# Kernel tuning notes

Measured on AMD Instinct MI355X. Metric: run time of the kernel, lower is better.

Reference implementation:

```python
import jax, jax.numpy as jnp
import numpy as np

VOCAB = 256
EMBED = 128
HIDDEN = 512
BATCH = 64
SEQ = 1024


def setup_inputs() -> dict:
    key = jax.random.key(0)
    ks = jax.random.split(key, 6)
    x = jax.random.randint(ks[0], (BATCH, SEQ), 0, VOCAB)
    hidden = jnp.zeros((BATCH, HIDDEN), dtype=jnp.float32)
    embedding = jax.random.normal(ks[1], (VOCAB, EMBED), dtype=jnp.float32)
    W_xh = jax.random.normal(ks[2], (EMBED, HIDDEN), dtype=jnp.float32) * 0.01
    W_hh = jax.random.normal(ks[3], (HIDDEN, HIDDEN), dtype=jnp.float32) * 0.01
    b_h = jnp.zeros((HIDDEN,), dtype=jnp.float32)
    # nn.Linear(hidden, vocab): weight [vocab, hidden], bias [vocab]
    W_hy_w = jax.random.normal(ks[4], (VOCAB, HIDDEN), dtype=jnp.float32) * (1.0 / np.sqrt(HIDDEN))
    W_hy_b = jax.random.normal(ks[5], (VOCAB,), dtype=jnp.float32) * 0.01
    return {"x": x, "hidden": hidden, "embedding": embedding, "W_xh": W_xh,
            "W_hh": W_hh, "b_h": b_h, "W_hy_w": W_hy_w, "W_hy_b": W_hy_b}


def reference(x, hidden, embedding, W_xh, W_hh, b_h, W_hy_w, W_hy_b):
    # x: [b, l] int tokens -> embed: [b, l, e]
    x_embed = embedding[x]
    # Precompute input projections in one batched GEMM: [l, b, h]
    xw = jnp.einsum('ble,eh->lbh', x_embed, W_xh) + b_h

    def step(h, xw_t):
        h_new = jnp.tanh(xw_t + h @ W_hh)
        return h_new, h_new

    final_hidden, outs = jax.lax.scan(step, hidden, xw)  # outs: [l, b, h]
    outs = jnp.transpose(outs, (1, 0, 2))  # [b, l, h]
    logits = outs @ W_hy_w.T + W_hy_b  # [b, l, vocab]
    return logits, final_hidden
```

## Files before the change

kernel.cpp:

```cpp
#include <hip/hip_runtime.h>
#include <hip/hip_bf16.h>
#include <stdint.h>

#define BATCH  64
#define SEQ    1024
#define EMBED  128
#define HIDDEN 512
#define VOCAB  256

using bf16 = __hip_bfloat16;
typedef __attribute__((ext_vector_type(8))) short bf16x8;
typedef __attribute__((ext_vector_type(4))) float f32x4;

__device__ __forceinline__ float bfu(unsigned short u) {
    return __uint_as_float(((unsigned)u) << 16);
}

__global__ void k_cvt(const float* __restrict__ in, bf16* __restrict__ out, int n) {
    int i = blockIdx.x * 256 + threadIdx.x;
    if (i < n) out[i] = __float2bfloat16(in[i]);
}

__global__ void k_txp_wxh(const float* __restrict__ in, bf16* __restrict__ out) {
    int idx = blockIdx.x * 256 + threadIdx.x;
    int e = idx >> 9, j = idx & 511;
    out[j * EMBED + e] = __float2bfloat16(in[idx]);
}

__global__ void k_txp_whh(const float* __restrict__ in, bf16* __restrict__ out) {
    int idx = blockIdx.x * 256 + threadIdx.x;
    int k = idx >> 9, n = idx & 511;
    out[n * HIDDEN + k] = __float2bfloat16(in[idx]);
}

template<bool GATHER, bool OUT_BF16>
__global__ __launch_bounds__(256) void k_gemm(
    const bf16* __restrict__ A,
    const int*  __restrict__ xtok,
    const bf16* __restrict__ B,
    const float* __restrict__ bias,
    float* __restrict__ Cf,
    bf16*  __restrict__ Cb,
    int M, int N, int K)
{
    __shared__ bf16 As[64][72];
    __shared__ bf16 Bs[64][72];
    const int m0 = blockIdx.x * 64, n0 = blockIdx.y * 64;
    const int tid  = threadIdx.x;
    const int lane = tid & 63, wid = tid >> 6;
    const int wm = wid >> 1, wn = wid & 1;
    const int lrow = tid >> 3, lc8 = tid & 7;

    f32x4 acc[2][2] = {};

    for (int k0 = 0; k0 < K; k0 += 64) {
#pragma unroll
        for (int pass = 0; pass < 2; ++pass) {
            int row = pass * 32 + lrow;
            const bf16* asrc;
            if (GATHER) {
                int m = m0 + row;
                int t = m >> 6, bb = m & 63;
                int tok = xtok[bb * SEQ + t];
                asrc = A + (size_t)tok * K + k0 + lc8 * 8;
            } else {
                asrc = A + (size_t)(m0 + row) * K + k0 + lc8 * 8;
            }
            *reinterpret_cast<uint4*>(&As[row][lc8 * 8]) = *reinterpret_cast<const uint4*>(asrc);
            *reinterpret_cast<uint4*>(&Bs[row][lc8 * 8]) =
                *reinterpret_cast<const uint4*>(B + (size_t)(n0 + row) * K + k0 + lc8 * 8);
        }
        __syncthreads();
#pragma unroll
        for (int kk = 0; kk < 2; ++kk) {
            bf16x8 af[2], bg[2];
#pragma unroll
            for (int mt = 0; mt < 2; ++mt)
                af[mt] = *reinterpret_cast<const bf16x8*>(
                    &As[wm * 32 + mt * 16 + (lane & 15)][kk * 32 + (lane >> 4) * 8]);
#pragma unroll
            for (int nt = 0; nt < 2; ++nt)
                bg[nt] = *reinterpret_cast<const bf16x8*>(
                    &Bs[wn * 32 + nt * 16 + (lane & 15)][kk * 32 + (lane >> 4) * 8]);
#pragma unroll
            for (int mt = 0; mt < 2; ++mt)
#pragma unroll
                for (int nt = 0; nt < 2; ++nt)
                    acc[mt][nt] = __builtin_amdgcn_mfma_f32_16x16x32_bf16(
                        af[mt], bg[nt], acc[mt][nt], 0, 0, 0);
        }
        __syncthreads();
    }
#pragma unroll
    for (int mt = 0; mt < 2; ++mt) {
        int rbase = m0 + wm * 32 + mt * 16 + (lane >> 4) * 4;
#pragma unroll
        for (int nt = 0; nt < 2; ++nt) {
            int col = n0 + wn * 32 + nt * 16 + (lane & 15);
            float bv = bias[col];
#pragma unroll
            for (int r = 0; r < 4; ++r) {
                float v = acc[mt][nt][r] + bv;
                size_t off = (size_t)(rbase + r) * N + col;
                if (OUT_BF16) Cb[off] = __float2bfloat16(v);
                else          Cf[off] = v;
            }
        }
    }
}

#define ROWS 16
#define CHK_LDS 3
#define CHK_REG 8
#define WRES_STRIDE (CHK_LDS * 32 + 8)
#define H_STRIDE (HIDDEN + 8)

__global__ __launch_bounds__(512, 2) void k_scan_mfma(
    const bf16* __restrict__ xwb,
    const bf16* __restrict__ wt,
    const float* __restrict__ h0,
    bf16* __restrict__ hh,
    float* __restrict__ hfin)
{
    __shared__ bf16 wres[HIDDEN * WRES_STRIDE];
    __shared__ bf16 h_lds[2][ROWS * H_STRIDE];

    const int tid  = threadIdx.x;
    const int lane = tid & 63, wid = tid >> 6;
    const int b0   = blockIdx.x * ROWS;
    const int scol = wid * 64;
    const int lm   = lane & 15, lk = lane >> 4;

    {
        const bf16* src = wt + (size_t)tid * HIDDEN;
        bf16* dst = &wres[tid * WRES_STRIDE];
#pragma unroll
        for (int j = 0; j < (CHK_LDS * 32) / 8; ++j)
            *reinterpret_cast<uint4*>(dst + j * 8) =
                *reinterpret_cast<const uint4*>(src + j * 8);
    }
    {
        int row = tid >> 5, c = (tid & 31) * 16;
        const float* src = h0 + (size_t)(b0 + row) * HIDDEN + c;
        bf16 tmp[16];
#pragma unroll
        for (int j = 0; j < 16; ++j) tmp[j] = __float2bfloat16(src[j]);
        *reinterpret_cast<uint4*>(&h_lds[0][row * H_STRIDE + c])     = *reinterpret_cast<uint4*>(&tmp[0]);
        *reinterpret_cast<uint4*>(&h_lds[0][row * H_STRIDE + c + 8]) = *reinterpret_cast<uint4*>(&tmp[8]);
    }

    bf16x8 breg[CHK_REG][4];
#pragma unroll
    for (int c = 0; c < CHK_REG; ++c)
#pragma unroll
        for (int nt = 0; nt < 4; ++nt)
            breg[c][nt] = *reinterpret_cast<const bf16x8*>(
                wt + (size_t)(scol + nt * 16 + lm) * HIDDEN + (CHK_LDS + c) * 32 + lk * 8);

    const bf16* grow[4];
    const bf16* lrow[4];
#pragma unroll
    for (int nt = 0; nt < 4; ++nt) {
        int row = scol + nt * 16 + lm;
        grow[nt] = wt + (size_t)row * HIDDEN + lk * 8;
        lrow[nt] = &wres[row * WRES_STRIDE + lk * 8];
    }

    __syncthreads();

    int p = 0;
    for (int t = 0; t < SEQ; ++t) {
        const ushort* xbase = reinterpret_cast<const ushort*>(
            xwb + ((size_t)t * BATCH + b0) * HIDDEN);
        ushort xwv[4][4];
#pragma unroll
        for (int nt = 0; nt < 4; ++nt)
#pragma unroll
            for (int r = 0; r < 4; ++r)
                xwv[nt][r] = xbase[(size_t)(lk * 4 + r) * HIDDEN + scol + nt * 16 + lm];

        f32x4 acc[4] = {};
#pragma unroll
        for (int kc = 0; kc < 16; ++kc) {
            bf16x8 af = *reinterpret_cast<const bf16x8*>(
                &h_lds[p][lm * H_STRIDE + kc * 32 + lk * 8]);
#pragma unroll
            for (int nt = 0; nt < 4; ++nt) {
                bf16x8 bg;
                if (kc < CHK_LDS)
                    bg = *reinterpret_cast<const bf16x8*>(lrow[nt] + kc * 32);
                else if (kc < CHK_LDS + CHK_REG)
                    bg = breg[kc - CHK_LDS][nt];
                else
                    bg = *reinterpret_cast<const bf16x8*>(grow[nt] + kc * 32);
                acc[nt] = __builtin_amdgcn_mfma_f32_16x16x32_bf16(af, bg, acc[nt], 0, 0, 0);
            }
        }

#pragma unroll
        for (int nt = 0; nt < 4; ++nt) {
            int col = scol + nt * 16 + lm;
#pragma unroll
            for (int r = 0; r < 4; ++r) {
                int m = lk * 4 + r;
                float pre = acc[nt][r] + bfu(xwv[nt][r]);
                float e2  = __expf(2.f * pre);
                float hn  = 1.f - 2.f / (e2 + 1.f);
                bf16 hb   = __float2bfloat16(hn);
                h_lds[p ^ 1][m * H_STRIDE + col] = hb;
                hh[((size_t)(b0 + m) * SEQ + t) * HIDDEN + col] = hb;
                if (t == SEQ - 1) hfin[(size_t)(b0 + m) * HIDDEN + col] = hn;
            }
        }
        p ^= 1;
        __syncthreads();
    }
}

extern "C" void kernel_launch(void* const* d_in, const int* in_sizes, int n_in,
                              void* d_out, int out_size, void* d_ws, size_t ws_size,
                              hipStream_t stream) {
    const int*   x    = (const int*)  d_in[0];
    const float* h0   = (const float*)d_in[1];
    const float* emb  = (const float*)d_in[2];
    const float* wxh  = (const float*)d_in[3];
    const float* whh  = (const float*)d_in[4];
    const float* bh   = (const float*)d_in[5];
    const float* whyw = (const float*)d_in[6];
    const float* whyb = (const float*)d_in[7];

    float* logits = (float*)d_out;
    float* hfin   = logits + (size_t)BATCH * SEQ * VOCAB;

    char* p = (char*)d_ws;
    bf16* xwb    = (bf16*)p; p += (size_t)SEQ * BATCH * HIDDEN * 2;
    bf16* hh     = (bf16*)p; p += (size_t)BATCH * SEQ * HIDDEN * 2;
    bf16* wt     = (bf16*)p; p += (size_t)HIDDEN * HIDDEN * 2;
    bf16* wxh_t  = (bf16*)p; p += (size_t)HIDDEN * EMBED * 2;
    bf16* emb_bf = (bf16*)p; p += (size_t)VOCAB * EMBED * 2;
    bf16* why_bf = (bf16*)p; p += (size_t)VOCAB * HIDDEN * 2;

    k_txp_whh<<<(HIDDEN * HIDDEN + 255) / 256, 256, 0, stream>>>(whh, wt);
    k_cvt<<<(VOCAB * EMBED + 255) / 256, 256, 0, stream>>>(emb, emb_bf, VOCAB * EMBED);
    k_cvt<<<(VOCAB * HIDDEN + 255) / 256, 256, 0, stream>>>(whyw, why_bf, VOCAB * HIDDEN);
    k_txp_wxh<<<(EMBED * HIDDEN + 255) / 256, 256, 0, stream>>>(wxh, wxh_t);

    k_gemm<true, true><<<dim3((SEQ * BATCH) / 64, HIDDEN / 64), 256, 0, stream>>>(
        emb_bf, x, wxh_t, bh, nullptr, xwb, SEQ * BATCH, HIDDEN, EMBED);

    k_scan_mfma<<<BATCH / ROWS, 512, 0, stream>>>(xwb, wt, h0, hh, hfin);

    k_gemm<false, false><<<dim3((BATCH * SEQ) / 64, VOCAB / 64), 256, 0, stream>>>(
        hh, nullptr, why_bf, whyb, logits, nullptr, BATCH * SEQ, VOCAB, HIDDEN);
}
```

Baseline: 3.171 ms.

## Permute xw layout for per-thread vector loads and defer coalesced hh stores

The input-projection GEMM now writes its bf16 output in a permuted layout, so each scan thread loads its 16 xw values with two 16-byte loads instead of 16 scattered 2-byte loads. The scan no longer stores each hidden element straight to global memory. Instead it copies the previous step's h from LDS to hh with wide coalesced stores at the start of the next step, plus one final flush after the loop. An empty asm barrier is also added to keep the register-resident weight chunks pinned. This targets the latency-bound serial recurrence by cutting per-step global memory instructions, at the cost of extra LDS reads and a layout tied to the fixed shapes.

```diff
diff --git a/kernel.cpp b/kernel.cpp
--- a/kernel.cpp
+++ b/kernel.cpp
@@ -33,7 +33,7 @@
     out[n * HIDDEN + k] = __float2bfloat16(in[idx]);
 }
 
-template<bool GATHER, bool OUT_BF16>
+template<bool GATHER, bool OUT_BF16, bool PERMUTE>
 __global__ __launch_bounds__(256) void k_gemm(
     const bf16* __restrict__ A,
     const int*  __restrict__ xtok,
@@ -91,19 +91,38 @@
         }
         __syncthreads();
     }
-#pragma unroll
-    for (int mt = 0; mt < 2; ++mt) {
-        int rbase = m0 + wm * 32 + mt * 16 + (lane >> 4) * 4;
-#pragma unroll
-        for (int nt = 0; nt < 2; ++nt) {
-            int col = n0 + wn * 32 + nt * 16 + (lane & 15);
-            float bv = bias[col];
-#pragma unroll
-            for (int r = 0; r < 4; ++r) {
-                float v = acc[mt][nt][r] + bv;
-                size_t off = (size_t)(rbase + r) * N + col;
-                if (OUT_BF16) Cb[off] = __float2bfloat16(v);
-                else          Cf[off] = v;
+    if (PERMUTE) {
+        const int t = m0 >> 6, wid_s = n0 >> 6;
+#pragma unroll
+        for (int mt = 0; mt < 2; ++mt) {
+            int blk = wm * 2 + mt;
+            bf16 tmp[8];
+#pragma unroll
+            for (int nt = 0; nt < 2; ++nt) {
+                int col = n0 + wn * 32 + nt * 16 + (lane & 15);
+                float bv = bias[col];
+#pragma unroll
+                for (int r = 0; r < 4; ++r)
+                    tmp[nt * 4 + r] = __float2bfloat16(acc[mt][nt][r] + bv);
+            }
+            size_t off = (((size_t)(t * 4 + blk) * 512) + wid_s * 64 + lane) * 16 + wn * 8;
+            *reinterpret_cast<uint4*>(Cb + off) = *reinterpret_cast<uint4*>(tmp);
+        }
+    } else {
+#pragma unroll
+        for (int mt = 0; mt < 2; ++mt) {
+            int rbase = m0 + wm * 32 + mt * 16 + (lane >> 4) * 4;
+#pragma unroll
+            for (int nt = 0; nt < 2; ++nt) {
+                int col = n0 + wn * 32 + nt * 16 + (lane & 15);
+                float bv = bias[col];
+#pragma unroll
+                for (int r = 0; r < 4; ++r) {
+                    float v = acc[mt][nt][r] + bv;
+                    size_t off = (size_t)(rbase + r) * N + col;
+                    if (OUT_BF16) Cb[off] = __float2bfloat16(v);
+                    else          Cf[off] = v;
+                }
             }
         }
     }
@@ -116,7 +135,7 @@
 #define H_STRIDE (HIDDEN + 8)
 
 __global__ __launch_bounds__(512, 2) void k_scan_mfma(
-    const bf16* __restrict__ xwb,
+    const bf16* __restrict__ xwp,
     const bf16* __restrict__ wt,
     const float* __restrict__ h0,
     bf16* __restrict__ hh,
@@ -153,31 +172,42 @@
 #pragma unroll
     for (int c = 0; c < CHK_REG; ++c)
 #pragma unroll
-        for (int nt = 0; nt < 4; ++nt)
+        for (int nt = 0; nt < 4; ++nt) {
             breg[c][nt] = *reinterpret_cast<const bf16x8*>(
                 wt + (size_t)(scol + nt * 16 + lm) * HIDDEN + (CHK_LDS + c) * 32 + lk * 8);
+            asm volatile("" : "+v"(breg[c][nt]));
+        }
 
     const bf16* grow[4];
-    const bf16* lrow[4];
+    const bf16* lrowp[4];
 #pragma unroll
     for (int nt = 0; nt < 4; ++nt) {
         int row = scol + nt * 16 + lm;
-        grow[nt] = wt + (size_t)row * HIDDEN + lk * 8;
-        lrow[nt] = &wres[row * WRES_STRIDE + lk * 8];
-    }
+        grow[nt]  = wt + (size_t)row * HIDDEN + lk * 8;
+        lrowp[nt] = &wres[row * WRES_STRIDE + lk * 8];
+    }
+
+    const int srow = tid >> 5, sc = (tid & 31) * 16;
 
     __syncthreads();
 
     int p = 0;
     for (int t = 0; t < SEQ; ++t) {
-        const ushort* xbase = reinterpret_cast<const ushort*>(
-            xwb + ((size_t)t * BATCH + b0) * HIDDEN);
-        ushort xwv[4][4];
-#pragma unroll
-        for (int nt = 0; nt < 4; ++nt)
-#pragma unroll
-            for (int r = 0; r < 4; ++r)
-                xwv[nt][r] = xbase[(size_t)(lk * 4 + r) * HIDDEN + scol + nt * 16 + lm];
+        if (t > 0) {
+            uint4 v0 = *reinterpret_cast<const uint4*>(&h_lds[p][srow * H_STRIDE + sc]);
+            uint4 v1 = *reinterpret_cast<const uint4*>(&h_lds[p][srow * H_STRIDE + sc + 8]);
+            bf16* dst = hh + ((size_t)(b0 + srow) * SEQ + (t - 1)) * HIDDEN + sc;
+            *reinterpret_cast<uint4*>(dst)     = v0;
+            *reinterpret_cast<uint4*>(dst + 8) = v1;
+        }
+
+        ushort xe[16];
+        {
+            const uint4* xp = reinterpret_cast<const uint4*>(xwp) +
+                              ((size_t)(t * 4 + blockIdx.x) * 512 + tid) * 2;
+            *reinterpret_cast<uint4*>(&xe[0]) = xp[0];
+            *reinterpret_cast<uint4*>(&xe[8]) = xp[1];
+        }
 
         f32x4 acc[4] = {};
 #pragma unroll
@@ -188,7 +218,7 @@
             for (int nt = 0; nt < 4; ++nt) {
                 bf16x8 bg;
                 if (kc < CHK_LDS)
-                    bg = *reinterpret_cast<const bf16x8*>(lrow[nt] + kc * 32);
+                    bg = *reinterpret_cast<const bf16x8*>(lrowp[nt] + kc * 32);
                 else if (kc < CHK_LDS + CHK_REG)
                     bg = breg[kc - CHK_LDS][nt];
                 else
@@ -203,17 +233,23 @@
 #pragma unroll
             for (int r = 0; r < 4; ++r) {
                 int m = lk * 4 + r;
-                float pre = acc[nt][r] + bfu(xwv[nt][r]);
+                float pre = acc[nt][r] + bfu(xe[nt * 4 + r]);
                 float e2  = __expf(2.f * pre);
                 float hn  = 1.f - 2.f / (e2 + 1.f);
-                bf16 hb   = __float2bfloat16(hn);
-                h_lds[p ^ 1][m * H_STRIDE + col] = hb;
-                hh[((size_t)(b0 + m) * SEQ + t) * HIDDEN + col] = hb;
+                h_lds[p ^ 1][m * H_STRIDE + col] = __float2bfloat16(hn);
                 if (t == SEQ - 1) hfin[(size_t)(b0 + m) * HIDDEN + col] = hn;
             }
         }
         p ^= 1;
         __syncthreads();
+    }
+
+    {
+        uint4 v0 = *reinterpret_cast<const uint4*>(&h_lds[p][srow * H_STRIDE + sc]);
+        uint4 v1 = *reinterpret_cast<const uint4*>(&h_lds[p][srow * H_STRIDE + sc + 8]);
+        bf16* dst = hh + ((size_t)(b0 + srow) * SEQ + (SEQ - 1)) * HIDDEN + sc;
+        *reinterpret_cast<uint4*>(dst)     = v0;
+        *reinterpret_cast<uint4*>(dst + 8) = v1;
     }
 }
 
@@ -233,7 +269,7 @@
     float* hfin   = logits + (size_t)BATCH * SEQ * VOCAB;
 
     char* p = (char*)d_ws;
-    bf16* xwb    = (bf16*)p; p += (size_t)SEQ * BATCH * HIDDEN * 2;
+    bf16* xwp    = (bf16*)p; p += (size_t)SEQ * BATCH * HIDDEN * 2;
     bf16* hh     = (bf16*)p; p += (size_t)BATCH * SEQ * HIDDEN * 2;
     bf16* wt     = (bf16*)p; p += (size_t)HIDDEN * HIDDEN * 2;
     bf16* wxh_t  = (bf16*)p; p += (size_t)HIDDEN * EMBED * 2;
@@ -245,11 +281,11 @@
     k_cvt<<<(VOCAB * HIDDEN + 255) / 256, 256, 0, stream>>>(whyw, why_bf, VOCAB * HIDDEN);
     k_txp_wxh<<<(EMBED * HIDDEN + 255) / 256, 256, 0, stream>>>(wxh, wxh_t);
 
-    k_gemm<true, true><<<dim3((SEQ * BATCH) / 64, HIDDEN / 64), 256, 0, stream>>>(
-        emb_bf, x, wxh_t, bh, nullptr, xwb, SEQ * BATCH, HIDDEN, EMBED);
-
-    k_scan_mfma<<<BATCH / ROWS, 512, 0, stream>>>(xwb, wt, h0, hh, hfin);
-
-    k_gemm<false, false><<<dim3((BATCH * SEQ) / 64, VOCAB / 64), 256, 0, stream>>>(
+    k_gemm<true, true, true><<<dim3((SEQ * BATCH) / 64, HIDDEN / 64), 256, 0, stream>>>(
+        emb_bf, x, wxh_t, bh, nullptr, xwp, SEQ * BATCH, HIDDEN, EMBED);
+
+    k_scan_mfma<<<BATCH / ROWS, 512, 0, stream>>>(xwp, wt, h0, hh, hfin);
+
+    k_gemm<false, false, false><<<dim3((BATCH * SEQ) / 64, VOCAB / 64), 256, 0, stream>>>(
         hh, nullptr, why_bf, whyb, logits, nullptr, BATCH * SEQ, VOCAB, HIDDEN);
 }
```

Measured after the change: 3.299 ms. 4.0% more time.
